# Optimization experiments

Measured on AMD Instinct MI355X. Metric: run time of the kernel, lower is better.

The kernel has to match this reference:

```python
import jax, jax.numpy as jnp
import numpy as np

B = 16          # graphs per batch
T = 50          # cell types
C = 200         # neurons per cell type
N = T * C       # nodes per graph (10000)
NT = B * N      # total nodes (160000)
FEAT = 1        # num_node_features (forced to 1 by module structure)
H = 8           # attention heads
DEG = 32
E = NT * DEG    # edges (5.12M)
PASSES = 4
PERSIST = 1.0
EPS = 1e-5
TAU = 1.0
SLOPE = 0.2


def setup_inputs() -> dict:
    key = jax.random.key(0)
    ks = jax.random.split(key, 12)
    x = jax.random.normal(ks[0], (NT, FEAT), dtype=jnp.float32)
    # sprinkle exact zeros so the noise-injection branch is exercised
    x = jnp.where(jax.random.uniform(ks[1], x.shape) < 0.1, 0.0, x)
    # edges stay within each graph (batched disjoint graphs)
    dst = jax.random.randint(ks[2], (E,), 0, NT)
    src = (dst // N) * N + jax.random.randint(ks[3], (E,), 0, N)
    edge_index = jnp.stack([src, dst]).astype(jnp.int32)
    batch = (jnp.arange(NT) // N).astype(jnp.int32)
    perm_weights = jax.random.normal(ks[4], (T, B, C, C), dtype=jnp.float32)
    decision_vec = (jax.random.uniform(ks[5], (N,)) < 0.2).astype(jnp.float32)
    gat_w = jax.random.normal(ks[6], (FEAT, H), dtype=jnp.float32)
    att_src = jax.random.normal(ks[7], (H,), dtype=jnp.float32)
    att_dst = jax.random.normal(ks[8], (H,), dtype=jnp.float32)
    return {
        "x": x, "edge_index": edge_index, "batch": batch,
        "perm_weights": perm_weights, "decision_vec": decision_vec,
        "gat_w": gat_w, "att_src": att_src, "att_dst": att_dst,
        "gat_bias": jnp.zeros((1,), jnp.float32),
        "bn_gamma": jnp.ones((1,), jnp.float32),
        "bn_beta": jnp.zeros((1,), jnp.float32),
        "bn_mean": jnp.zeros((1,), jnp.float32),
        "bn_var": jnp.ones((1,), jnp.float32),
        "lin_w": jax.random.normal(ks[9], (1, 1), dtype=jnp.float32),
        "lin_b": jax.random.normal(ks[10], (1,), dtype=jnp.float32),
    }


def _permutation_layer(x, perm_weights, key):
    # x: [NT, FEAT] -> per-type blocks [T, B, C, FEAT]
    xb = x.reshape(B, T, C, FEAT).transpose(1, 0, 2, 3)
    u = jax.random.uniform(key, perm_weights.shape, minval=1e-10, maxval=1.0)
    gumbel = -jnp.log(-jnp.log(u))
    # F.gumbel_softmax(weights, dim=1) on [B,C,C] -> softmax over row axis (axis=2 here)
    soft = jax.nn.softmax((perm_weights + gumbel) / TAU, axis=2)
    y = jnp.einsum('tbij,tbjf->tbif', soft, xb)
    return y.transpose(1, 0, 2, 3).reshape(NT, FEAT)


def _add_noise(x, key):
    nz = x != 0
    n = nz.sum().astype(x.dtype)
    mean = jnp.sum(jnp.where(nz, x, 0.0)) / n
    var = jnp.sum(jnp.where(nz, (x - mean) ** 2, 0.0)) / (n - 1.0)  # unbiased, as torch .std()
    std = jnp.sqrt(var)
    noise = (std / 100.0) * jax.random.normal(key, x.shape, dtype=x.dtype)
    return jnp.where(nz, x, noise)


def _gat_conv(x, src, dst, gat_w, att_src, att_dst, gat_bias):
    xs = x @ gat_w                                   # [NT, H] (out_channels=1 per head)
    a_src = xs * att_src                             # [NT, H]
    a_dst = xs * att_dst
    e = a_src[src] + a_dst[dst]                      # [E+NT, H]
    e = jnp.where(e > 0, e, SLOPE * e)               # leaky_relu(0.2)
    emax = jax.ops.segment_max(e, dst, num_segments=NT)
    ee = jnp.exp(e - emax[dst])
    denom = jax.ops.segment_sum(ee, dst, num_segments=NT)
    alpha = ee / denom[dst]
    out = jax.ops.segment_sum(alpha * xs[src], dst, num_segments=NT)  # [NT, H]
    return out.mean(axis=1, keepdims=True) + gat_bias  # concat=False -> mean over heads


def reference(x, edge_index, batch, perm_weights, decision_vec, gat_w, att_src,
              att_dst, gat_bias, bn_gamma, bn_beta, bn_mean, bn_var, lin_w, lin_b):
    rk = jax.random.key(42)
    x = _permutation_layer(x, perm_weights, jax.random.fold_in(rk, 0))
    x_res = x
    x = _add_noise(x, jax.random.fold_in(rk, 1))
    # GATConv adds self loops by default
    loops = jnp.arange(NT, dtype=edge_index.dtype)
    src = jnp.concatenate([edge_index[0], loops])
    dst = jnp.concatenate([edge_index[1], loops])
    for i in range(PASSES):
        x = _gat_conv(x, src, dst, gat_w, att_src, att_dst, gat_bias)
        x = (x - bn_mean) / jnp.sqrt(bn_var + EPS) * bn_gamma + bn_beta  # eval BN
        x = jax.nn.silu(x)
        # dropout is identity in eval mode
        x = x + x_res * (PERSIST ** i)
    mask = jnp.tile(decision_vec, B)[:, None]        # [NT, 1]
    x = x * mask
    pooled = jax.ops.segment_max(x, batch, num_segments=B)  # global_max_pool -> [B, 1]
    return jax.nn.relu(pooled @ lin_w.T + lin_b)
```

## Files before the change

kernel.cpp:

```cpp
#include <hip/hip_runtime.h>
#include <stdint.h>
#include <math.h>

#define B_   16
#define T_   50
#define C_   200
#define N_   10000
#define NT_  160000
#define H_   8
#define E_   5120000
#define EPS_ 1e-5f
#define NB_  625
#define EB_  512
#define EPB_ 10000
#define ATH_ 1024
#define GB_  40
#define GC_  250
#define JC_  5
#define JW_  40
#define ROWP_ 41
#define LOG2E_ 1.44269504088896340736f

__device__ __forceinline__ float ex2(float x){
  float r; asm("v_exp_f32 %0, %1" : "=v"(r) : "v"(x)); return r;
}

struct TF2C { unsigned a, b; };
constexpr unsigned rotl32c(unsigned v, int r){ return (v << r) | (v >> (32 - r)); }
constexpr TF2C tf_const(unsigned k0, unsigned k1, unsigned x0, unsigned x1){
  unsigned ks2 = k0 ^ k1 ^ 0x1BD11BDAu;
  unsigned ks[3] = {k0, k1, ks2};
  x0 += k0; x1 += k1;
  const int RA[4] = {13, 15, 26, 6};
  const int RB[4] = {17, 29, 16, 24};
  for (int g = 0; g < 5; ++g){
    for (int r = 0; r < 4; ++r){
      int rr = (g & 1) ? RB[r] : RA[r];
      x0 += x1; x1 = rotl32c(x1, rr); x1 ^= x0;
    }
    x0 += ks[(g + 1) % 3];
    x1 += ks[(g + 2) % 3] + (unsigned)(g + 1);
  }
  return TF2C{x0, x1};
}
constexpr TF2C KG = tf_const(0u, 42u, 0u, 0u);
constexpr TF2C KN = tf_const(0u, 42u, 0u, 1u);

__device__ __forceinline__ void tf2(unsigned k0, unsigned k1, unsigned x0, unsigned x1,
                                    unsigned &o0, unsigned &o1){
  unsigned ks2 = k0 ^ k1 ^ 0x1BD11BDAu;
  x0 += k0; x1 += k1;
#define TFR_(R) { x0 += x1; x1 = __builtin_rotateleft32(x1, R); x1 ^= x0; }
  TFR_(13) TFR_(15) TFR_(26) TFR_(6)  x0 += k1;  x1 += ks2 + 1u;
  TFR_(17) TFR_(29) TFR_(16) TFR_(24) x0 += ks2; x1 += k0 + 2u;
  TFR_(13) TFR_(15) TFR_(26) TFR_(6)  x0 += k0;  x1 += k1 + 3u;
  TFR_(17) TFR_(29) TFR_(16) TFR_(24) x0 += k1;  x1 += ks2 + 4u;
  TFR_(13) TFR_(15) TFR_(26) TFR_(6)  x0 += ks2; x1 += k0 + 5u;
#undef TFR_
  o0 = x0; o1 = x1;
}
__device__ __forceinline__ unsigned rbits(unsigned ka, unsigned kb, unsigned m){
  unsigned a, b; tf2(ka, kb, 0u, m, a, b); return a ^ b;
}

__device__ __forceinline__ float erfinv_xla(float x){
  float w = -log1pf(-x * x);
  float p;
  if (w < 5.0f){
    w = w - 2.5f;
    p = 2.81022636e-08f;
    p = fmaf(p, w, 3.43273939e-07f);
    p = fmaf(p, w, -3.5233877e-06f);
    p = fmaf(p, w, -4.39150654e-06f);
    p = fmaf(p, w, 0.00021858087f);
    p = fmaf(p, w, -0.00125372503f);
    p = fmaf(p, w, -0.00417768164f);
    p = fmaf(p, w, 0.246640727f);
    p = fmaf(p, w, 1.50140941f);
  } else {
    w = sqrtf(w) - 3.0f;
    p = -0.000200214257f;
    p = fmaf(p, w, 0.000100950558f);
    p = fmaf(p, w, 0.00134934322f);
    p = fmaf(p, w, -0.00367342844f);
    p = fmaf(p, w, 0.00573950773f);
    p = fmaf(p, w, -0.0076224613f);
    p = fmaf(p, w, 0.00943887047f);
    p = fmaf(p, w, 1.00167406f);
    p = fmaf(p, w, 2.83297682f);
  }
  return p * x;
}

__global__ __launch_bounds__(ATH_)
void k_hist(const int* __restrict__ dst, int* __restrict__ cnt){
  __shared__ int h[NB_];
  int tid = threadIdx.x, blk = blockIdx.x;
  for (int i = tid; i < NB_; i += ATH_) h[i] = 0;
  __syncthreads();
  int e0 = blk * EPB_;
  for (int i = tid; i < EPB_; i += ATH_)
    atomicAdd(&h[dst[e0 + i] >> 8], 1);
  __syncthreads();
  for (int i = tid; i < NB_; i += ATH_) cnt[blk * NB_ + i] = h[i];
}

__global__ __launch_bounds__(512)
void k_sumb(const int* __restrict__ cnt, int* __restrict__ bsum){
  __shared__ int sred[8];
  int b = blockIdx.x, tid = threadIdx.x;
  int v = cnt[tid * NB_ + b];
#pragma unroll
  for (int s = 32; s >= 1; s >>= 1) v += __shfl_xor(v, s, 64);
  int w = tid >> 6, l = tid & 63;
  if (l == 0) sred[w] = v;
  __syncthreads();
  if (tid == 0){
    int t = 0;
#pragma unroll
    for (int i = 0; i < 8; ++i) t += sred[i];
    bsum[b] = t;
  }
}

__global__ void k_scanb(const int* __restrict__ bsum, int* __restrict__ boff){
  __shared__ int ts[256];
  int tid = threadIdx.x;
  int i0 = tid * 3;
  int c0 = (i0 + 0 < NB_) ? bsum[i0 + 0] : 0;
  int c1 = (i0 + 1 < NB_) ? bsum[i0 + 1] : 0;
  int c2 = (i0 + 2 < NB_) ? bsum[i0 + 2] : 0;
  int s = c0 + c1 + c2;
  ts[tid] = s;
  __syncthreads();
  for (int d = 1; d < 256; d <<= 1){
    int t = (tid >= d) ? ts[tid - d] : 0;
    __syncthreads();
    ts[tid] += t;
    __syncthreads();
  }
  int run = ts[tid] - s;
  if (i0 + 0 <= NB_){ boff[i0 + 0] = run; run += c0; }
  if (i0 + 1 <= NB_){ boff[i0 + 1] = run; run += c1; }
  if (i0 + 2 <= NB_){ boff[i0 + 2] = run; run += c2; }
}

__global__ __launch_bounds__(512)
void k_scanc(const int* __restrict__ cnt, const int* __restrict__ boff,
             int* __restrict__ gscan){
  __shared__ int ts[512];
  int b = blockIdx.x, tid = threadIdx.x;
  int v = cnt[tid * NB_ + b];
  ts[tid] = v;
  __syncthreads();
  for (int d = 1; d < 512; d <<= 1){
    int t = (tid >= d) ? ts[tid - d] : 0;
    __syncthreads();
    ts[tid] += t;
    __syncthreads();
  }
  gscan[tid * NB_ + b] = boff[b] + ts[tid] - v;
}

__global__ __launch_bounds__(ATH_)
void k_append(const int* __restrict__ src, const int* __restrict__ dst,
              const int* __restrict__ gscan, unsigned* __restrict__ ebuf){
  __shared__ unsigned esh[EPB_];
  __shared__ int hist[NB_];
  __shared__ int loff[NB_ + 1];
  int tid = threadIdx.x, blk = blockIdx.x;
  int e0 = blk * EPB_;
  for (int i = tid; i < NB_; i += ATH_) hist[i] = 0;
  __syncthreads();
  for (int i = tid; i < EPB_; i += ATH_)
    atomicAdd(&hist[dst[e0 + i] >> 8], 1);
  __syncthreads();
  if (tid < NB_) loff[tid + 1] = hist[tid];
  if (tid == 0) loff[0] = 0;
  __syncthreads();
  for (int d = 1; d < NB_; d <<= 1){
    int v = 0;
    if (tid < NB_ && tid >= d) v = loff[tid + 1 - d];
    __syncthreads();
    if (tid < NB_ && tid >= d) loff[tid + 1] += v;
    __syncthreads();
  }
  for (int i = tid; i < NB_; i += ATH_) hist[i] = 0;
  __syncthreads();
  for (int i = tid; i < EPB_; i += ATH_){
    int e = e0 + i;
    int d = dst[e];
    int b = d >> 8;
    int p = loff[b] + atomicAdd(&hist[b], 1);
    esh[p] = ((unsigned)src[e] << 8) | (unsigned)(d & 255);
  }
  __syncthreads();
  int wv = tid >> 6, ln = tid & 63;
  for (int b = wv; b < NB_; b += ATH_ / 64){
    int lo = loff[b], len = loff[b + 1] - lo;
    int gb0 = gscan[blk * NB_ + b];
    for (int p = ln; p < len; p += 64)
      ebuf[gb0 + p] = esh[lo + p];
  }
}

__global__ __launch_bounds__(256)
void k_bcsr(const int* __restrict__ boff, const unsigned* __restrict__ ebuf,
            int* __restrict__ offs, unsigned short* __restrict__ srcs16){
  __shared__ int cnt[256];
  __shared__ int ts[256];
  int b = blockIdx.x, tid = threadIdx.x;
  int e0 = boff[b], e1 = boff[b + 1];
  int base_node = b * 256;
  int offA = (base_node / N_) * N_;
  int boundary = offA + N_;
  cnt[tid] = 0;
  __syncthreads();
  for (int e = e0 + tid; e < e1; e += 256)
    atomicAdd(&cnt[ebuf[e] & 255u], 1);
  __syncthreads();
  int v = cnt[tid];
  ts[tid] = v;
  __syncthreads();
  for (int d = 1; d < 256; d <<= 1){
    int t = (tid >= d) ? ts[tid - d] : 0;
    __syncthreads();
    ts[tid] += t;
    __syncthreads();
  }
  int excl = ts[tid] - v;
  offs[base_node + tid] = e0 + excl;
  __syncthreads();
  cnt[tid] = excl;
  __syncthreads();
  for (int e = e0 + tid; e < e1; e += 256){
    unsigned pk = ebuf[e];
    int dl = (int)(pk & 255u);
    int goff = (base_node + dl >= boundary) ? boundary : offA;
    int pos = e0 + atomicAdd(&cnt[dl], 1);
    srcs16[pos] = (unsigned short)((int)(pk >> 8) - goff);
  }
  if (b == 0 && tid == 0) offs[NT_] = E_;
}

__global__ __launch_bounds__(512, 8)
void k_perm(const float* __restrict__ W, const float* __restrict__ x,
            float* __restrict__ ypart){
  __shared__ float ez[C_ * ROWP_];
  __shared__ float Ssh[JW_];
  __shared__ float rs[JW_];

  const int bid = blockIdx.x;
  const int tb = bid / JC_;
  const int jc = bid - tb * JC_;
  const int t = tb / B_;
  const int b = tb - t * B_;
  const int j0 = jc * JW_;
  const int xoff = (b * T_ + t) * C_;
  const int tid = threadIdx.x;
  const int w = tid >> 6, l = tid & 63;

  {
    int i = tid / JW_;
    int jj = tid - i * JW_;
    unsigned m = (unsigned)(tb * (C_ * C_) + i * C_ + j0 + jj);
    int la = i * ROWP_ + jj;
    int niter = (C_ * JW_ - tid + 511) >> 9;
    for (int it = 0; it < niter; ++it){
      unsigned bits = rbits(KG.a, KG.b, m);
      float f = __uint_as_float((bits >> 9) | 0x3f800000u) - 1.0f;
      float tneg;
      if (f >= 0.875f){
        float d = 1.0f - f;
        float p = 0.16666667f;
        p = fmaf(p, d, 0.2f);
        p = fmaf(p, d, 0.25f);
        p = fmaf(p, d, 0.33333333f);
        p = fmaf(p, d, 0.5f);
        p = fmaf(p, d, 1.0f);
        tneg = d * p;
      } else {
        float u = f + 1e-10f;
        tneg = -__logf(u);
      }
      ez[la] = __expf(W[m]) * __builtin_amdgcn_rcpf(tneg);
      jj += 32;
      int wrap = jj >= JW_;
      jj = wrap ? jj - JW_ : jj;
      m += wrap ? 2592u : 2432u;
      la += wrap ? 525 : 524;
    }
  }
  __syncthreads();

#pragma unroll
  for (int q = 0; q < 5; ++q){
    int jj = w * 5 + q;
    float s = ez[l * ROWP_ + jj] + ez[(l + 64) * ROWP_ + jj] + ez[(l + 128) * ROWP_ + jj]
            + ((l < 8) ? ez[(l + 192) * ROWP_ + jj] : 0.f);
#pragma unroll
    for (int sh = 32; sh >= 1; sh >>= 1) s += __shfl_xor(s, sh, 64);
    if (l == 0) Ssh[jj] = s;
  }
  __syncthreads();
  if (tid < JW_) rs[tid] = x[xoff + j0 + tid] / Ssh[tid];
  __syncthreads();

  if (tid < C_){
    float acc = 0.f;
#pragma unroll 8
    for (int jj = 0; jj < JW_; ++jj)
      acc = fmaf(ez[tid * ROWP_ + jj], rs[jj], acc);
    ypart[jc * NT_ + xoff + tid] = acc;
  }
}

__global__ __launch_bounds__(256)
void k_ycomb(const float* __restrict__ ypart, float* __restrict__ y,
             float* __restrict__ spart){
  __shared__ float sred[12];
  int n = blockIdx.x * 256 + threadIdx.x;
  float v = 0.f;
#pragma unroll
  for (int jc = 0; jc < JC_; ++jc) v += ypart[jc * NT_ + n];
  y[n] = v;
  float s = 0.f, c = 0.f, q = 0.f;
  if (v != 0.f){ s = v; c = 1.f; q = v * v; }
#pragma unroll
  for (int sh = 32; sh >= 1; sh >>= 1){
    s += __shfl_xor(s, sh, 64);
    c += __shfl_xor(c, sh, 64);
    q += __shfl_xor(q, sh, 64);
  }
  int w = threadIdx.x >> 6, l = threadIdx.x & 63;
  if (l == 0){ sred[w] = s; sred[4 + w] = c; sred[8 + w] = q; }
  __syncthreads();
  if (threadIdx.x == 0){
    spart[blockIdx.x * 3 + 0] = sred[0] + sred[1] + sred[2] + sred[3];
    spart[blockIdx.x * 3 + 1] = sred[4] + sred[5] + sred[6] + sred[7];
    spart[blockIdx.x * 3 + 2] = sred[8] + sred[9] + sred[10] + sred[11];
  }
}

__global__ void k_stat2(const float* __restrict__ spart, float* __restrict__ stats){
  __shared__ float sred[12];
  int tid = threadIdx.x;
  float s = 0.f, c = 0.f, q = 0.f;
  for (int i = tid; i < 625; i += 256){
    s += spart[i * 3 + 0];
    c += spart[i * 3 + 1];
    q += spart[i * 3 + 2];
  }
#pragma unroll
  for (int sh = 32; sh >= 1; sh >>= 1){
    s += __shfl_xor(s, sh, 64);
    c += __shfl_xor(c, sh, 64);
    q += __shfl_xor(q, sh, 64);
  }
  int w = tid >> 6, l = tid & 63;
  if (l == 0){ sred[w] = s; sred[4 + w] = c; sred[8 + w] = q; }
  __syncthreads();
  if (tid == 0){
    float S = sred[0] + sred[1] + sred[2] + sred[3];
    float C = sred[4] + sred[5] + sred[6] + sred[7];
    float Q = sred[8] + sred[9] + sred[10] + sred[11];
    float var = (Q - S * S / C) / (C - 1.f);
    stats[0] = sqrtf(var) * 0.01f;
  }
}

__global__ void k_noise(const float* __restrict__ y, const float* __restrict__ stats,
                        float* __restrict__ x0){
  int n = blockIdx.x * 256 + threadIdx.x;
  float v = y[n];
  if (v != 0.0f){ x0[n] = v; return; }
  float scale = stats[0];
  unsigned bits = rbits(KN.a, KN.b, (unsigned)n);
  float f = __uint_as_float((bits >> 9) | 0x3f800000u) - 1.0f;
  float u = f * 2.0f + (-0.99999994f);
  u = fmaxf(-0.99999994f, u);
  float nrm = 1.41421356237f * erfinv_xla(u);
  x0[n] = scale * nrm;
}

__global__ __launch_bounds__(256)
void k_gat(const float* __restrict__ xin, const float* __restrict__ xres,
           const int* __restrict__ offs, const unsigned short* __restrict__ srcs16,
           const float* __restrict__ gw, const float* __restrict__ asrc,
           const float* __restrict__ adst, const float* __restrict__ gbias,
           const float* __restrict__ bng, const float* __restrict__ bnb,
           const float* __restrict__ bnm, const float* __restrict__ bnv,
           float* __restrict__ xout){
  __shared__ float xsh[N_];
  int g = blockIdx.x / GB_, c = blockIdx.x - g * GB_;
  int tid = threadIdx.x;
  const float4* xv = (const float4*)(xin + g * N_);
  for (int i = tid; i < N_ / 4; i += 256) ((float4*)xsh)[i] = xv[i];
  __syncthreads();
  if (tid >= GC_) return;

  int nl = c * GC_ + tid;
  int n = g * N_ + nl;
  float xn = xsh[nl];

  float cs[H_], cdxn[H_], wv[H_];
#pragma unroll
  for (int h = 0; h < H_; ++h){
    wv[h] = gw[h];
    cs[h] = wv[h] * asrc[h] * LOG2E_;
    cdxn[h] = wv[h] * adst[h] * xn * LOG2E_;
  }
  float mh[H_], den[H_], num[H_];
#pragma unroll
  for (int h = 0; h < H_; ++h){
    float v = cs[h] * xn + cdxn[h];
    v = fmaxf(v, 0.2f * v);
    mh[h] = v; den[h] = 1.f; num[h] = xn;
  }
  int e0 = offs[n], e1 = offs[n + 1];
  for (int e = e0; e < e1; ++e){
    float xs = xsh[srcs16[e]];
#pragma unroll
    for (int h = 0; h < H_; ++h){
      float v = fmaf(cs[h], xs, cdxn[h]);
      v = fmaxf(v, 0.2f * v);
      float d = v - mh[h];
      float ed = ex2(-fabsf(d));
      bool newmax = d > 0.f;
      float corr = newmax ? ed : 1.f;
      float p    = newmax ? 1.f : ed;
      mh[h] = newmax ? v : mh[h];
      den[h] = fmaf(den[h], corr, p);
      num[h] = fmaf(num[h], corr, p * xs);
    }
  }
  float o = 0.f;
#pragma unroll
  for (int h = 0; h < H_; ++h) o += wv[h] * num[h] * __builtin_amdgcn_rcpf(den[h]);
  o = o * 0.125f + gbias[0];
  o = (o - bnm[0]) / sqrtf(bnv[0] + EPS_) * bng[0] + bnb[0];
  o = o / (1.0f + __expf(-o));
  xout[n] = o + xres[n];
}

__global__ __launch_bounds__(256)
void k_pool1(const float* __restrict__ xf, const float* __restrict__ dv,
             float* __restrict__ pmax){
  __shared__ float sred[4];
  int g = blockIdx.x / GB_, c = blockIdx.x - g * GB_;
  int tid = threadIdx.x;
  float m = -INFINITY;
  if (tid < GC_){
    int nl = c * GC_ + tid;
    m = xf[g * N_ + nl] * dv[nl];
  }
#pragma unroll
  for (int s = 32; s >= 1; s >>= 1) m = fmaxf(m, __shfl_xor(m, s, 64));
  int w = tid >> 6, l = tid & 63;
  if (l == 0) sred[w] = m;
  __syncthreads();
  if (tid == 0)
    pmax[blockIdx.x] = fmaxf(fmaxf(sred[0], sred[1]), fmaxf(sred[2], sred[3]));
}

__global__ void k_pool2(const float* __restrict__ pmax, const float* __restrict__ lw,
                        const float* __restrict__ lb, float* __restrict__ out){
  int b = blockIdx.x, l = threadIdx.x;
  float m = (l < GB_) ? pmax[b * GB_ + l] : -INFINITY;
#pragma unroll
  for (int s = 32; s >= 1; s >>= 1) m = fmaxf(m, __shfl_xor(m, s, 64));
  if (l == 0){
    float o = m * lw[0] + lb[0];
    out[b] = (o > 0.f) ? o : 0.f;
  }
}

extern "C" void kernel_launch(void* const* d_in, const int* in_sizes, int n_in,
                              void* d_out, int out_size, void* d_ws, size_t ws_size,
                              hipStream_t stream){
  const float* x     = (const float*)d_in[0];
  const int*   ei    = (const int*)d_in[1];
  const float* W     = (const float*)d_in[3];
  const float* dv    = (const float*)d_in[4];
  const float* gw    = (const float*)d_in[5];
  const float* asrc  = (const float*)d_in[6];
  const float* adst  = (const float*)d_in[7];
  const float* gbias = (const float*)d_in[8];
  const float* bng   = (const float*)d_in[9];
  const float* bnb   = (const float*)d_in[10];
  const float* bnm   = (const float*)d_in[11];
  const float* bnv   = (const float*)d_in[12];
  const float* lw    = (const float*)d_in[13];
  const float* lb    = (const float*)d_in[14];
  float* out = (float*)d_out;

  char* ws = (char*)d_ws;
  int*            offs   = (int*)           (ws + 0);
  unsigned short* srcs16 = (unsigned short*)(ws + 640256);
  int*            cnt    = (int*)           (ws + 10880256);
  int*            gscan  = (int*)           (ws + 12160256);
  unsigned*       ebuf   = (unsigned*)      (ws + 21120256);
  float*          ypart  = (float*)         (ws + 21120256);
  float*          y      = (float*)         (ws + 41600256);
  float*          x0     = (float*)         (ws + 42240256);
  float*          x1     = (float*)         (ws + 42880256);
  int*            bsum   = (int*)           (ws + 43520256);
  int*            boff   = (int*)           (ws + 43522816);
  float*          pmax   = (float*)         (ws + 43525376);
  float*          stats  = (float*)         (ws + 43527936);
  float*          spart  = (float*)         (ws + 43527968);
  if (ws_size < (size_t)43535500) return;

  const int* esrc = ei;
  const int* edst = ei + E_;

  k_hist  <<<EB_, ATH_, 0, stream>>>(edst, cnt);
  k_sumb  <<<NB_, 512, 0, stream>>>(cnt, bsum);
  k_scanb <<<1, 256, 0, stream>>>(bsum, boff);
  k_scanc <<<NB_, 512, 0, stream>>>(cnt, boff, gscan);
  k_append<<<EB_, ATH_, 0, stream>>>(esrc, edst, gscan, ebuf);
  k_bcsr  <<<NB_, 256, 0, stream>>>(boff, ebuf, offs, srcs16);
  k_perm  <<<T_ * B_ * JC_, 512, 0, stream>>>(W, x, ypart);
  k_ycomb <<<625, 256, 0, stream>>>(ypart, y, spart);
  k_stat2 <<<1, 256, 0, stream>>>(spart, stats);
  k_noise <<<625, 256, 0, stream>>>(y, stats, x0);
  k_gat<<<B_ * GB_, 256, 0, stream>>>(x0, y, offs, srcs16, gw, asrc, adst, gbias, bng, bnb, bnm, bnv, x1);
  k_gat<<<B_ * GB_, 256, 0, stream>>>(x1, y, offs, srcs16, gw, asrc, adst, gbias, bng, bnb, bnm, bnv, x0);
  k_gat<<<B_ * GB_, 256, 0, stream>>>(x0, y, offs, srcs16, gw, asrc, adst, gbias, bng, bnb, bnm, bnv, x1);
  k_gat<<<B_ * GB_, 256, 0, stream>>>(x1, y, offs, srcs16, gw, asrc, adst, gbias, bng, bnb, bnm, bnv, x0);
  k_pool1 <<<B_ * GB_, 256, 0, stream>>>(x0, dv, pmax);
  k_pool2 <<<B_, 64, 0, stream>>>(pmax, lw, lb, out);
}
```

Before: 325.9 us.

## Use wave-shuffle scans, reuse histogram counts, widen GAT blocks, cheaper RNG transcendentals

Replaces the shared-memory Hillis-Steele scans in scanb, scanc, append and bcsr with wavefront shuffle scans, which removes many block-wide barriers. k_append now reads the per-block bucket histogram already computed by k_hist instead of recomputing it with atomics. The GAT and pooling kernels move to 512-thread blocks with half as many blocks, so each block loads the graph's features into shared memory fewer times. The permutation kernel uses raw v_log/v_exp and integer-domain comparisons for the gumbel noise. The changes touch several unrelated kernels, and the larger GAT blocks may reduce occupancy and parallelism.

```diff
diff --git a/kernel.cpp b/kernel.cpp
--- a/kernel.cpp
+++ b/kernel.cpp
@@ -14,8 +14,8 @@
 #define EB_  512
 #define EPB_ 10000
 #define ATH_ 1024
-#define GB_  40
-#define GC_  250
+#define GB_  20
+#define GC_  500
 #define JC_  5
 #define JW_  40
 #define ROWP_ 41
@@ -23,6 +23,18 @@
 
 __device__ __forceinline__ float ex2(float x){
   float r; asm("v_exp_f32 %0, %1" : "=v"(r) : "v"(x)); return r;
+}
+__device__ __forceinline__ float lg2(float x){
+  float r; asm("v_log_f32 %0, %1" : "=v"(r) : "v"(x)); return r;
+}
+
+__device__ __forceinline__ int wscan_incl(int v, int lane){
+#pragma unroll
+  for (int d = 1; d < 64; d <<= 1){
+    int t = __shfl_up(v, d, 64);
+    if (lane >= d) v += t;
+  }
+  return v;
 }
 
 struct TF2C { unsigned a, b; };
@@ -123,121 +135,111 @@
   }
 }
 
-__global__ void k_scanb(const int* __restrict__ bsum, int* __restrict__ boff){
-  __shared__ int ts[256];
-  int tid = threadIdx.x;
-  int i0 = tid * 3;
-  int c0 = (i0 + 0 < NB_) ? bsum[i0 + 0] : 0;
-  int c1 = (i0 + 1 < NB_) ? bsum[i0 + 1] : 0;
-  int c2 = (i0 + 2 < NB_) ? bsum[i0 + 2] : 0;
-  int s = c0 + c1 + c2;
-  ts[tid] = s;
-  __syncthreads();
-  for (int d = 1; d < 256; d <<= 1){
-    int t = (tid >= d) ? ts[tid - d] : 0;
-    __syncthreads();
-    ts[tid] += t;
-    __syncthreads();
-  }
-  int run = ts[tid] - s;
-  if (i0 + 0 <= NB_){ boff[i0 + 0] = run; run += c0; }
-  if (i0 + 1 <= NB_){ boff[i0 + 1] = run; run += c1; }
-  if (i0 + 2 <= NB_){ boff[i0 + 2] = run; run += c2; }
+__global__ __launch_bounds__(640)
+void k_scanb(const int* __restrict__ bsum, int* __restrict__ boff){
+  __shared__ int wsum[16];
+  int tid = threadIdx.x, lane = tid & 63, wid = tid >> 6;
+  int v = (tid < NB_) ? bsum[tid] : 0;
+  int inc = wscan_incl(v, lane);
+  if (lane == 63) wsum[wid] = inc;
+  __syncthreads();
+  if (wid == 0){
+    int wv = (lane < 10) ? wsum[lane] : 0;
+    int wi = wscan_incl(wv, lane);
+    if (lane < 10) wsum[lane] = wi - wv;
+  }
+  __syncthreads();
+  if (tid < NB_) boff[tid] = inc - v + wsum[wid];
+  if (tid == 0) boff[NB_] = E_;
 }
 
 __global__ __launch_bounds__(512)
 void k_scanc(const int* __restrict__ cnt, const int* __restrict__ boff,
              int* __restrict__ gscan){
-  __shared__ int ts[512];
-  int b = blockIdx.x, tid = threadIdx.x;
+  __shared__ int wsum[8];
+  int b = blockIdx.x, tid = threadIdx.x, lane = tid & 63, wid = tid >> 6;
   int v = cnt[tid * NB_ + b];
-  ts[tid] = v;
-  __syncthreads();
-  for (int d = 1; d < 512; d <<= 1){
-    int t = (tid >= d) ? ts[tid - d] : 0;
-    __syncthreads();
-    ts[tid] += t;
-    __syncthreads();
-  }
-  gscan[tid * NB_ + b] = boff[b] + ts[tid] - v;
+  int inc = wscan_incl(v, lane);
+  if (lane == 63) wsum[wid] = inc;
+  __syncthreads();
+  int wp = 0;
+#pragma unroll
+  for (int k = 0; k < 8; ++k) wp += (k < wid) ? wsum[k] : 0;
+  gscan[tid * NB_ + b] = boff[b] + inc - v + wp;
 }
 
 __global__ __launch_bounds__(ATH_)
 void k_append(const int* __restrict__ src, const int* __restrict__ dst,
-              const int* __restrict__ gscan, unsigned* __restrict__ ebuf){
+              const int* __restrict__ cnt, const int* __restrict__ gscan,
+              unsigned* __restrict__ ebuf){
   __shared__ unsigned esh[EPB_];
-  __shared__ int hist[NB_];
   __shared__ int loff[NB_ + 1];
+  __shared__ int cur[NB_];
+  __shared__ int wsum[16];
   int tid = threadIdx.x, blk = blockIdx.x;
+  int lane = tid & 63, wid = tid >> 6;
   int e0 = blk * EPB_;
-  for (int i = tid; i < NB_; i += ATH_) hist[i] = 0;
-  __syncthreads();
-  for (int i = tid; i < EPB_; i += ATH_)
-    atomicAdd(&hist[dst[e0 + i] >> 8], 1);
-  __syncthreads();
-  if (tid < NB_) loff[tid + 1] = hist[tid];
-  if (tid == 0) loff[0] = 0;
-  __syncthreads();
-  for (int d = 1; d < NB_; d <<= 1){
-    int v = 0;
-    if (tid < NB_ && tid >= d) v = loff[tid + 1 - d];
-    __syncthreads();
-    if (tid < NB_ && tid >= d) loff[tid + 1] += v;
-    __syncthreads();
-  }
-  for (int i = tid; i < NB_; i += ATH_) hist[i] = 0;
+  for (int i = tid; i < NB_; i += ATH_) cur[i] = 0;
+  int hv = (tid < NB_) ? cnt[blk * NB_ + tid] : 0;
+  int inc = wscan_incl(hv, lane);
+  if (lane == 63 && wid < 10) wsum[wid] = inc;
+  __syncthreads();
+  if (wid == 0){
+    int wv = (lane < 10) ? wsum[lane] : 0;
+    int wi = wscan_incl(wv, lane);
+    if (lane < 10) wsum[lane] = wi - wv;
+  }
+  __syncthreads();
+  if (tid < NB_) loff[tid] = inc - hv + wsum[wid];
+  if (tid == 0) loff[NB_] = EPB_;
   __syncthreads();
   for (int i = tid; i < EPB_; i += ATH_){
     int e = e0 + i;
     int d = dst[e];
     int b = d >> 8;
-    int p = loff[b] + atomicAdd(&hist[b], 1);
+    int p = loff[b] + atomicAdd(&cur[b], 1);
     esh[p] = ((unsigned)src[e] << 8) | (unsigned)(d & 255);
   }
   __syncthreads();
-  int wv = tid >> 6, ln = tid & 63;
-  for (int b = wv; b < NB_; b += ATH_ / 64){
+  for (int b = wid; b < NB_; b += ATH_ / 64){
     int lo = loff[b], len = loff[b + 1] - lo;
     int gb0 = gscan[blk * NB_ + b];
-    for (int p = ln; p < len; p += 64)
+    for (int p = lane; p < len; p += 64)
       ebuf[gb0 + p] = esh[lo + p];
   }
 }
 
-__global__ __launch_bounds__(256)
+__global__ __launch_bounds__(512)
 void k_bcsr(const int* __restrict__ boff, const unsigned* __restrict__ ebuf,
             int* __restrict__ offs, unsigned short* __restrict__ srcs16){
   __shared__ int cnt[256];
-  __shared__ int ts[256];
-  int b = blockIdx.x, tid = threadIdx.x;
+  __shared__ int cur[256];
+  __shared__ int wsum[4];
+  int b = blockIdx.x, tid = threadIdx.x, lane = tid & 63, wid = tid >> 6;
   int e0 = boff[b], e1 = boff[b + 1];
   int base_node = b * 256;
   int offA = (base_node / N_) * N_;
   int boundary = offA + N_;
-  cnt[tid] = 0;
-  __syncthreads();
-  for (int e = e0 + tid; e < e1; e += 256)
+  if (tid < 256) cnt[tid] = 0;
+  __syncthreads();
+  for (int e = e0 + tid; e < e1; e += 512)
     atomicAdd(&cnt[ebuf[e] & 255u], 1);
   __syncthreads();
-  int v = cnt[tid];
-  ts[tid] = v;
-  __syncthreads();
-  for (int d = 1; d < 256; d <<= 1){
-    int t = (tid >= d) ? ts[tid - d] : 0;
-    __syncthreads();
-    ts[tid] += t;
-    __syncthreads();
-  }
-  int excl = ts[tid] - v;
-  offs[base_node + tid] = e0 + excl;
-  __syncthreads();
-  cnt[tid] = excl;
-  __syncthreads();
-  for (int e = e0 + tid; e < e1; e += 256){
+  int v = (tid < 256) ? cnt[tid] : 0;
+  int inc = wscan_incl(v, lane);
+  if (lane == 63 && wid < 4) wsum[wid] = inc;
+  __syncthreads();
+  int wp = 0;
+#pragma unroll
+  for (int k = 0; k < 4; ++k) wp += (k < wid) ? wsum[k] : 0;
+  int excl = inc - v + wp;
+  if (tid < 256){ offs[base_node + tid] = e0 + excl; cur[tid] = excl; }
+  __syncthreads();
+  for (int e = e0 + tid; e < e1; e += 512){
     unsigned pk = ebuf[e];
     int dl = (int)(pk & 255u);
     int goff = (base_node + dl >= boundary) ? boundary : offA;
-    int pos = e0 + atomicAdd(&cnt[dl], 1);
+    int pos = e0 + atomicAdd(&cur[dl], 1);
     srcs16[pos] = (unsigned short)((int)(pk >> 8) - goff);
   }
   if (b == 0 && tid == 0) offs[NT_] = E_;
@@ -268,10 +270,10 @@
     int niter = (C_ * JW_ - tid + 511) >> 9;
     for (int it = 0; it < niter; ++it){
       unsigned bits = rbits(KG.a, KG.b, m);
-      float f = __uint_as_float((bits >> 9) | 0x3f800000u) - 1.0f;
+      float fc = (float)(bits >> 9);
       float tneg;
-      if (f >= 0.875f){
-        float d = 1.0f - f;
+      if (bits >= 0xFC000000u){
+        float d = fmaf(-fc, 0x1p-23f, 1.0f);
         float p = 0.16666667f;
         p = fmaf(p, d, 0.2f);
         p = fmaf(p, d, 0.25f);
@@ -280,10 +282,10 @@
         p = fmaf(p, d, 1.0f);
         tneg = d * p;
       } else {
-        float u = f + 1e-10f;
-        tneg = -__logf(u);
+        float u = fmaf(fc, 0x1p-23f, 1e-10f);
+        tneg = lg2(u) * -0.69314718056f;
       }
-      ez[la] = __expf(W[m]) * __builtin_amdgcn_rcpf(tneg);
+      ez[la] = ex2(W[m] * LOG2E_) * __builtin_amdgcn_rcpf(tneg);
       jj += 32;
       int wrap = jj >= JW_;
       jj = wrap ? jj - JW_ : jj;
@@ -383,7 +385,7 @@
   x0[n] = scale * nrm;
 }
 
-__global__ __launch_bounds__(256)
+__global__ __launch_bounds__(512)
 void k_gat(const float* __restrict__ xin, const float* __restrict__ xres,
            const int* __restrict__ offs, const unsigned short* __restrict__ srcs16,
            const float* __restrict__ gw, const float* __restrict__ asrc,
@@ -395,7 +397,7 @@
   int g = blockIdx.x / GB_, c = blockIdx.x - g * GB_;
   int tid = threadIdx.x;
   const float4* xv = (const float4*)(xin + g * N_);
-  for (int i = tid; i < N_ / 4; i += 256) ((float4*)xsh)[i] = xv[i];
+  for (int i = tid; i < N_ / 4; i += 512) ((float4*)xsh)[i] = xv[i];
   __syncthreads();
   if (tid >= GC_) return;
 
@@ -443,10 +445,10 @@
   xout[n] = o + xres[n];
 }
 
-__global__ __launch_bounds__(256)
+__global__ __launch_bounds__(512)
 void k_pool1(const float* __restrict__ xf, const float* __restrict__ dv,
              float* __restrict__ pmax){
-  __shared__ float sred[4];
+  __shared__ float sred[8];
   int g = blockIdx.x / GB_, c = blockIdx.x - g * GB_;
   int tid = threadIdx.x;
   float m = -INFINITY;
@@ -459,8 +461,12 @@
   int w = tid >> 6, l = tid & 63;
   if (l == 0) sred[w] = m;
   __syncthreads();
-  if (tid == 0)
-    pmax[blockIdx.x] = fmaxf(fmaxf(sred[0], sred[1]), fmaxf(sred[2], sred[3]));
+  if (tid == 0){
+    float p = sred[0];
+#pragma unroll
+    for (int i = 1; i < 8; ++i) p = fmaxf(p, sred[i]);
+    pmax[blockIdx.x] = p;
+  }
 }
 
 __global__ void k_pool2(const float* __restrict__ pmax, const float* __restrict__ lw,
@@ -516,18 +522,18 @@
 
   k_hist  <<<EB_, ATH_, 0, stream>>>(edst, cnt);
   k_sumb  <<<NB_, 512, 0, stream>>>(cnt, bsum);
-  k_scanb <<<1, 256, 0, stream>>>(bsum, boff);
+  k_scanb <<<1, 640, 0, stream>>>(bsum, boff);
   k_scanc <<<NB_, 512, 0, stream>>>(cnt, boff, gscan);
-  k_append<<<EB_, ATH_, 0, stream>>>(esrc, edst, gscan, ebuf);
-  k_bcsr  <<<NB_, 256, 0, stream>>>(boff, ebuf, offs, srcs16);
+  k_append<<<EB_, ATH_, 0, stream>>>(esrc, edst, cnt, gscan, ebuf);
+  k_bcsr  <<<NB_, 512, 0, stream>>>(boff, ebuf, offs, srcs16);
   k_perm  <<<T_ * B_ * JC_, 512, 0, stream>>>(W, x, ypart);
   k_ycomb <<<625, 256, 0, stream>>>(ypart, y, spart);
   k_stat2 <<<1, 256, 0, stream>>>(spart, stats);
   k_noise <<<625, 256, 0, stream>>>(y, stats, x0);
-  k_gat<<<B_ * GB_, 256, 0, stream>>>(x0, y, offs, srcs16, gw, asrc, adst, gbias, bng, bnb, bnm, bnv, x1);
-  k_gat<<<B_ * GB_, 256, 0, stream>>>(x1, y, offs, srcs16, gw, asrc, adst, gbias, bng, bnb, bnm, bnv, x0);
-  k_gat<<<B_ * GB_, 256, 0, stream>>>(x0, y, offs, srcs16, gw, asrc, adst, gbias, bng, bnb, bnm, bnv, x1);
-  k_gat<<<B_ * GB_, 256, 0, stream>>>(x1, y, offs, srcs16, gw, asrc, adst, gbias, bng, bnb, bnm, bnv, x0);
-  k_pool1 <<<B_ * GB_, 256, 0, stream>>>(x0, dv, pmax);
+  k_gat<<<B_ * GB_, 512, 0, stream>>>(x0, y, offs, srcs16, gw, asrc, adst, gbias, bng, bnb, bnm, bnv, x1);
+  k_gat<<<B_ * GB_, 512, 0, stream>>>(x1, y, offs, srcs16, gw, asrc, adst, gbias, bng, bnb, bnm, bnv, x0);
+  k_gat<<<B_ * GB_, 512, 0, stream>>>(x0, y, offs, srcs16, gw, asrc, adst, gbias, bng, bnb, bnm, bnv, x1);
+  k_gat<<<B_ * GB_, 512, 0, stream>>>(x1, y, offs, srcs16, gw, asrc, adst, gbias, bng, bnb, bnm, bnv, x0);
+  k_pool1 <<<B_ * GB_, 512, 0, stream>>>(x0, dv, pmax);
   k_pool2 <<<B_, 64, 0, stream>>>(pmax, lw, lb, out);
 }
```

Result: slower. 343.7 us (+5.5%).
